# Optimization experiments

Hardware: AMD Instinct MI355X
Metric: run time of the kernel (lower is better)

Reference implementation:

```python
import jax, jax.numpy as jnp
import numpy as np

N_NODES = 50000
N_EDGES = 800000
DIM_FEAT = 96
INFO_DIM = 32
DIM_EMB = 160
CONV_OUT = DIM_EMB - INFO_DIM  # 128
NUM_LAYERS = 3
NUM_GRAPHS = 500
DIM_TARGET = 10


def setup_inputs() -> dict:
    key = jax.random.key(0)
    ks = jax.random.split(key, 20)
    inp = {
        'x': jax.random.normal(ks[0], (N_NODES, DIM_FEAT), dtype=jnp.float32),
        'edge_index': jax.random.randint(ks[1], (2, N_EDGES), 0, N_NODES, dtype=jnp.int32),
        'batch': jnp.sort(jax.random.randint(ks[2], (N_NODES,), 0, NUM_GRAPHS, dtype=jnp.int32)),
        'struc_info': jax.random.normal(ks[3], (NUM_GRAPHS, INFO_DIM), dtype=jnp.float32),
    }
    # SAGEConv params per layer: lin_l (on aggregated neighbors, with bias), lin_r (on root, no bias)
    in_dims = [DIM_FEAT + INFO_DIM, DIM_EMB, DIM_EMB]
    k = 4
    for i, din in enumerate(in_dims):
        s = 1.0 / np.sqrt(din)
        inp[f'Wl{i}'] = jax.random.uniform(ks[k], (din, CONV_OUT), jnp.float32, -s, s); k += 1
        inp[f'Wr{i}'] = jax.random.uniform(ks[k], (din, CONV_OUT), jnp.float32, -s, s); k += 1
        inp[f'b{i}'] = jax.random.uniform(ks[k], (CONV_OUT,), jnp.float32, -s, s); k += 1
    s1 = 1.0 / np.sqrt(NUM_LAYERS * CONV_OUT)
    inp['Wfc1'] = jax.random.uniform(ks[k], (NUM_LAYERS * CONV_OUT, DIM_EMB), jnp.float32, -s1, s1); k += 1
    inp['bfc1'] = jax.random.uniform(ks[k], (DIM_EMB,), jnp.float32, -s1, s1); k += 1
    s2 = 1.0 / np.sqrt(DIM_EMB)
    inp['Wfc2'] = jax.random.uniform(ks[k], (DIM_EMB, DIM_TARGET), jnp.float32, -s2, s2); k += 1
    inp['bfc2'] = jax.random.uniform(ks[k], (DIM_TARGET,), jnp.float32, -s2, s2)
    return inp


def _sage_conv(h, src, dst, Wl, Wr, b, n_nodes):
    # PyG SAGEConv (mean aggr): out = lin_l(mean_{j in N(i)} x_j) + lin_r(x_i)
    agg = jax.ops.segment_sum(h[src], dst, num_segments=n_nodes)       # [N, D]
    deg = jax.ops.segment_sum(jnp.ones_like(dst, dtype=h.dtype), dst, num_segments=n_nodes)
    mean = agg / jnp.maximum(deg, 1.0)[:, None]
    return mean @ Wl + b + h @ Wr


def reference(x, edge_index, batch, struc_info, Wl0, Wr0, b0, Wl1, Wr1, b1, Wl2, Wr2, b2, Wfc1, bfc1, Wfc2, bfc2):
    n_nodes = x.shape[0]
    src, dst = edge_index[0], edge_index[1]
    info = struc_info[batch]                         # [N, info_dim] repeated per node
    params = [(Wl0, Wr0, b0), (Wl1, Wr1, b1), (Wl2, Wr2, b2)]
    h = x
    outs = []
    for (Wl, Wr, b) in params:
        h = _sage_conv(jnp.concatenate([h, info], axis=1), src, dst, Wl, Wr, b, n_nodes)
        outs.append(h)
    hcat = jnp.concatenate(outs, axis=1)             # [N, num_layers*conv_out]
    g = jax.ops.segment_max(hcat, batch, num_segments=struc_info.shape[0])  # global max pool
    z = jax.nn.relu(g @ Wfc1 + bfc1)
    return z @ Wfc2 + bfc2
```

## Files before the change

### kernel.cpp

```cpp
#include <hip/hip_runtime.h>
#include <hip/hip_bf16.h>
#include <float.h>

#define NN 50000
#define NE 800000
#define DF 96
#define DI 32
#define CO 128
#define NG 500
#define HC 384
#define F1I 384
#define F1O 160
#define F2O 10
#define CAPLOG 7
#define NRANGE 196
#define EPB 3125
#define RCAPLOG 13

typedef unsigned int  u32;
typedef unsigned short u16;
typedef short bf16x8 __attribute__((ext_vector_type(8)));
typedef float f32x4  __attribute__((ext_vector_type(4)));

__device__ __forceinline__ u16 f2b(float f) {
    __hip_bfloat16 h = __float2bfloat16(f);
    return *reinterpret_cast<u16*>(&h);
}
__device__ __forceinline__ float b2f(u16 u) {
    return __uint_as_float(((u32)u) << 16);
}
__device__ __forceinline__ float blo(u32 u) { return __uint_as_float(u << 16); }
__device__ __forceinline__ float bhi(u32 u) { return __uint_as_float(u & 0xffff0000u); }

#define PB_BIN    256
#define PB_STARTS 196
#define PB_CAST   4688
#define PB_WT0    96
#define PB_WT1    128
#define PB_WT2    128
#define PB_INFO   500
#define PREP_GRID (PB_BIN + PB_STARTS + PB_CAST + PB_WT0 + PB_WT1 + PB_WT2 + 3 * PB_INFO)

__global__ __launch_bounds__(256) void k_prep(
        const float* __restrict__ x, const int* __restrict__ batch, const float* __restrict__ info,
        const int* __restrict__ src, const int* __restrict__ dst,
        const float* __restrict__ Wl0, const float* __restrict__ Wr0, const float* __restrict__ b0,
        const float* __restrict__ Wl1, const float* __restrict__ Wr1, const float* __restrict__ b1,
        const float* __restrict__ Wl2, const float* __restrict__ Wr2, const float* __restrict__ b2,
        int* __restrict__ grescnt, u32* __restrict__ ebin,
        int* __restrict__ start, u16* __restrict__ xb,
        u16* __restrict__ WT0, u16* __restrict__ WT1, u16* __restrict__ WT2,
        float* __restrict__ iQl0, float* __restrict__ iQr0,
        float* __restrict__ iQl1, float* __restrict__ iQr1,
        float* __restrict__ iQl2, float* __restrict__ iQr2) {
    __shared__ u32 pairs[EPB];
    __shared__ int lcnt[256];
    int blk = blockIdx.x;
    int t = threadIdx.x;
    if (blk < PB_BIN) {
        int base = blk * EPB;
        lcnt[t] = 0;
        __syncthreads();
        for (int j = t; j < EPB; j += 256) {
            int e = base + j;
            int d = dst[e];
            int s = src[e];
            pairs[j] = ((u32)(d & 255) << 24) | ((u32)(d >> 8) << 16) | (u32)s;
            atomicAdd(&lcnt[d >> 8], 1);
        }
        __syncthreads();
        int myCnt = lcnt[t];
        int myBase = atomicAdd(&grescnt[t * 16], myCnt);
        __syncthreads();
        lcnt[t] = myBase;
        __syncthreads();
        for (int j = t; j < EPB; j += 256) {
            u32 p = pairs[j];
            int r = (p >> 16) & 255;
            int pos = atomicAdd(&lcnt[r], 1);
            if (pos < (1 << RCAPLOG)) ebin[(r << RCAPLOG) + pos] = p;
        }
        return;
    }
    blk -= PB_BIN;
    if (blk < PB_STARTS) {
        int i = blk * 256 + t;
        if (i >= NN) return;
        int b = batch[i];
        if (i == 0) { for (int g = 0; g <= b; ++g) start[g] = 0; }
        else {
            int p = batch[i - 1];
            if (p != b) for (int g = p + 1; g <= b; ++g) start[g] = i;
        }
        if (i == NN - 1) { for (int g = b + 1; g <= NG; ++g) start[g] = NN; }
        return;
    }
    blk -= PB_STARTS;
    if (blk < PB_CAST) {
        int tid = blk * 256 + t;
        if (tid >= NN * DF / 4) return;
        float4 v = *(const float4*)&x[tid * 4];
        ushort4 o;
        o.x = f2b(v.x); o.y = f2b(v.y); o.z = f2b(v.z); o.w = f2b(v.w);
        *(ushort4*)&xb[tid * 4] = o;
        return;
    }
    blk -= PB_CAST;
    if (blk < PB_WT0 + PB_WT1 + PB_WT2) {
        const float* Wl; const float* Wr; u16* WT; int K; int rel;
        if (blk < PB_WT0) { Wl = Wl0; Wr = Wr0; WT = WT0; K = 96;  rel = blk; }
        else if (blk < PB_WT0 + PB_WT1) { Wl = Wl1; Wr = Wr1; WT = WT1; K = 128; rel = blk - PB_WT0; }
        else { Wl = Wl2; Wr = Wr2; WT = WT2; K = 128; rel = blk - PB_WT0 - PB_WT1; }
        int tid = rel * 256 + t;
        if (tid >= 256 * K) return;
        int n = tid / K;
        int k = tid - n * K;
        float v = (n < CO) ? Wl[k * CO + n] : Wr[k * CO + (n - CO)];
        WT[tid] = f2b(v);
        return;
    }
    blk -= PB_WT0 + PB_WT1 + PB_WT2;
    {
        const float* Wl; const float* Wr; const float* bias; float* iQl; float* iQr; int Ktop; int g;
        if (blk < PB_INFO) { Wl = Wl0; Wr = Wr0; bias = b0; iQl = iQl0; iQr = iQr0; Ktop = 96;  g = blk; }
        else if (blk < 2 * PB_INFO) { Wl = Wl1; Wr = Wr1; bias = b1; iQl = iQl1; iQr = iQr1; Ktop = 128; g = blk - PB_INFO; }
        else { Wl = Wl2; Wr = Wr2; bias = b2; iQl = iQl2; iQr = iQr2; Ktop = 128; g = blk - 2 * PB_INFO; }
        int c = t & 127;
        int sel = t >> 7;
        const float* W = sel ? Wr : Wl;
        float a = sel ? bias[c] : 0.0f;
        for (int d = 0; d < DI; ++d)
            a += info[g * DI + d] * W[(Ktop + d) * CO + c];
        (sel ? iQr : iQl)[g * CO + c] = a;
    }
}

__global__ __launch_bounds__(256) void k_binB(const u32* __restrict__ ebin,
                                              const int* __restrict__ grescnt,
                                              int* __restrict__ cnt, u16* __restrict__ csr) {
    __shared__ int lcnt[256];
    int r = blockIdx.x;
    int t = threadIdx.x;
    lcnt[t] = 0;
    __syncthreads();
    int total = grescnt[r * 16];
    if (total > (1 << RCAPLOG)) total = 1 << RCAPLOG;
    for (int j = t; j < total; j += 256) {
        u32 p = ebin[(r << RCAPLOG) + j];
        int dloc = p >> 24;
        int rank = atomicAdd(&lcnt[dloc], 1);
        int node = (r << 8) + dloc;
        if (rank < (1 << CAPLOG)) csr[(node << CAPLOG) + rank] = (u16)(p & 0xffff);
    }
    __syncthreads();
    int node = (r << 8) + t;
    if (node < NN) cnt[node] = lcnt[t];
}

template<int K>
__global__ __launch_bounds__(256) void k_mfma(const u16* __restrict__ A,
                                              const u16* __restrict__ WTg,
                                              const int* __restrict__ batch,
                                              const float* __restrict__ iQl,
                                              const float* __restrict__ iQr,
                                              u16* __restrict__ zlp,
                                              u16* __restrict__ zq) {
    constexpr int PITCH = K + 8;
    __shared__ short lds[256 * PITCH];

    int tid  = threadIdx.x;
    int w    = tid >> 6;
    int lane = tid & 63;
    int quad = lane >> 4;
    int l15  = lane & 15;

    constexpr int CH = 256 * K / 8;
    const uint4* wp = (const uint4*)WTg;
    for (int c = tid; c < CH; c += 256) {
        int n  = c / (K / 8);
        int ko = (c - n * (K / 8)) * 8;
        *(uint4*)&lds[n * PITCH + ko] = wp[c];
    }
    __syncthreads();

    int i0 = blockIdx.x * 128 + w * 32;
    int r0 = i0 + l15;       if (r0 >= NN) r0 = NN - 1;
    int r1 = i0 + 16 + l15;  if (r1 >= NN) r1 = NN - 1;
    const short* A0 = (const short*)A + (size_t)r0 * K;
    const short* A1 = (const short*)A + (size_t)r1 * K;

    f32x4 acc[2][16];
#pragma unroll
    for (int rt = 0; rt < 2; ++rt)
#pragma unroll
        for (int ct = 0; ct < 16; ++ct)
            acc[rt][ct] = (f32x4){0.f, 0.f, 0.f, 0.f};

#pragma unroll
    for (int ks = 0; ks < K / 32; ++ks) {
        int ka = ks * 32 + quad * 8;
        bf16x8 a0 = *(const bf16x8*)(A0 + ka);
        bf16x8 a1 = *(const bf16x8*)(A1 + ka);
#pragma unroll
        for (int ct = 0; ct < 16; ++ct) {
            bf16x8 b = *(const bf16x8*)&lds[(ct * 16 + l15) * PITCH + ka];
            acc[0][ct] = __builtin_amdgcn_mfma_f32_16x16x32_bf16(a0, b, acc[0][ct], 0, 0, 0);
            acc[1][ct] = __builtin_amdgcn_mfma_f32_16x16x32_bf16(a1, b, acc[1][ct], 0, 0, 0);
        }
    }

#pragma unroll
    for (int rt = 0; rt < 2; ++rt) {
#pragma unroll
        for (int reg = 0; reg < 4; ++reg) {
            int row = i0 + rt * 16 + quad * 4 + reg;
            if (row < NN) {
                int b = batch[row];
                const float* ql = &iQl[b * CO];
                const float* qr = &iQr[b * CO];
                u16* lp = zlp + (size_t)row * CO;
                u16* qp = zq  + (size_t)row * CO;
#pragma unroll
                for (int ct = 0; ct < 8; ++ct) {
                    int col = ct * 16 + l15;
                    lp[col] = f2b(acc[rt][ct][reg] + ql[col]);
                }
#pragma unroll
                for (int ct = 8; ct < 16; ++ct) {
                    int col = ct * 16 + l15 - 128;
                    qp[col] = f2b(acc[rt][ct][reg] + qr[col]);
                }
            }
        }
    }
}

__device__ __forceinline__ void acc8(float* a, const uint4& u) {
    a[0] += blo(u.x); a[1] += bhi(u.x);
    a[2] += blo(u.y); a[3] += bhi(u.y);
    a[4] += blo(u.z); a[5] += bhi(u.z);
    a[6] += blo(u.w); a[7] += bhi(u.w);
}

__global__ __launch_bounds__(256) void k_gatherb(const u32* __restrict__ zlp, const u32* __restrict__ zq,
                                                 const int* __restrict__ cnt, const u16* __restrict__ csr,
                                                 u32* __restrict__ hout) {
    int wave = threadIdx.x >> 6;
    int lane = threadIdx.x & 63;
    int q    = lane >> 4;
    int l16  = lane & 15;
    int i = blockIdx.x * 4 + wave;
    if (i >= NN) return;
    int deg = cnt[i];
    int degc = min(deg, 1 << CAPLOG);
    int s0 = i << CAPLOG;
    int s1 = s0 + degc;

    const uint4* Z = (const uint4*)zlp;

    float a[8] = {0,0,0,0,0,0,0,0};
    float b[8] = {0,0,0,0,0,0,0,0};
    float c[8] = {0,0,0,0,0,0,0,0};
    float d[8] = {0,0,0,0,0,0,0,0};

    int e = s0;
    for (; e + 15 < s1; e += 16) {
        int n0 = csr[e + q];
        int n1 = csr[e + 4 + q];
        int n2 = csr[e + 8 + q];
        int n3 = csr[e + 12 + q];
        uint4 u0 = Z[(size_t)n0 * 16 + l16];
        uint4 u1 = Z[(size_t)n1 * 16 + l16];
        uint4 u2 = Z[(size_t)n2 * 16 + l16];
        uint4 u3 = Z[(size_t)n3 * 16 + l16];
        acc8(a, u0); acc8(b, u1); acc8(c, u2); acc8(d, u3);
    }
    for (; e < s1; e += 4) {
        if (e + q < s1) {
            int n0 = csr[e + q];
            uint4 u0 = Z[(size_t)n0 * 16 + l16];
            acc8(a, u0);
        }
    }
#pragma unroll
    for (int j = 0; j < 8; ++j) {
        a[j] += b[j] + c[j] + d[j];
        a[j] += __shfl_xor(a[j], 16);
        a[j] += __shfl_xor(a[j], 32);
    }
    if (q == 0) {
        float r = 1.0f / fmaxf((float)deg, 1.0f);
        uint4 qq = ((const uint4*)zq)[(size_t)i * 16 + l16];
        uint4 o;
        o.x = (u32)f2b(a[0] * r + blo(qq.x)) | ((u32)f2b(a[1] * r + bhi(qq.x)) << 16);
        o.y = (u32)f2b(a[2] * r + blo(qq.y)) | ((u32)f2b(a[3] * r + bhi(qq.y)) << 16);
        o.z = (u32)f2b(a[4] * r + blo(qq.z)) | ((u32)f2b(a[5] * r + bhi(qq.z)) << 16);
        o.w = (u32)f2b(a[6] * r + blo(qq.w)) | ((u32)f2b(a[7] * r + bhi(qq.w)) << 16);
        ((uint4*)hout)[(size_t)i * 16 + l16] = o;
    }
}

__global__ __launch_bounds__(384) void k_poolfc(const u32* __restrict__ h1, const u32* __restrict__ h2,
                                                const u32* __restrict__ h3, const int* __restrict__ start,
                                                const float* __restrict__ W1, const float* __restrict__ b1,
                                                const float* __restrict__ W2, const float* __restrict__ b2,
                                                float* __restrict__ out) {
    __shared__ float s_part[6][128];
    __shared__ float s_g[F1I];
    __shared__ float s_z[F1O];
    int gr = blockIdx.x;
    int t  = threadIdx.x;
    int w    = t >> 6;
    int lane = t & 63;
    int buf  = w % 3;
    int half = w / 3;
    const u32* hb = (buf == 0) ? h1 : (buf == 1) ? h2 : h3;
    int s = start[gr], e = start[gr + 1];
    int mid = (s + e) >> 1;
    int n0 = half ? mid : s;
    int n1 = half ? e : mid;

    float mlo[4], mhi[4];
#pragma unroll
    for (int j = 0; j < 4; ++j) { mlo[j] = -FLT_MAX; mhi[j] = -FLT_MAX; }
    int n = n0;
    for (; n + 3 < n1; n += 4) {
        u32 v0 = hb[(size_t)(n + 0) * 64 + lane];
        u32 v1 = hb[(size_t)(n + 1) * 64 + lane];
        u32 v2 = hb[(size_t)(n + 2) * 64 + lane];
        u32 v3 = hb[(size_t)(n + 3) * 64 + lane];
        mlo[0] = fmaxf(mlo[0], blo(v0)); mhi[0] = fmaxf(mhi[0], bhi(v0));
        mlo[1] = fmaxf(mlo[1], blo(v1)); mhi[1] = fmaxf(mhi[1], bhi(v1));
        mlo[2] = fmaxf(mlo[2], blo(v2)); mhi[2] = fmaxf(mhi[2], bhi(v2));
        mlo[3] = fmaxf(mlo[3], blo(v3)); mhi[3] = fmaxf(mhi[3], bhi(v3));
    }
    for (; n < n1; ++n) {
        u32 v0 = hb[(size_t)n * 64 + lane];
        mlo[0] = fmaxf(mlo[0], blo(v0)); mhi[0] = fmaxf(mhi[0], bhi(v0));
    }
    float lo = fmaxf(fmaxf(mlo[0], mlo[1]), fmaxf(mlo[2], mlo[3]));
    float hi = fmaxf(fmaxf(mhi[0], mhi[1]), fmaxf(mhi[2], mhi[3]));
    s_part[w][2 * lane]     = lo;
    s_part[w][2 * lane + 1] = hi;
    __syncthreads();
    {
        int buf2 = t >> 7, cc = t & 127;
        s_g[t] = fmaxf(s_part[buf2][cc], s_part[buf2 + 3][cc]);
    }
    __syncthreads();
    if (t < F1O) {
        float acc = b1[t];
        for (int k = 0; k < F1I; ++k) acc += s_g[k] * W1[k * F1O + t];
        s_z[t] = fmaxf(acc, 0.0f);
    }
    __syncthreads();
    if (t < F2O) {
        float a = b2[t];
        for (int k = 0; k < F1O; ++k) a += s_z[k] * W2[k * F2O + t];
        out[gr * F2O + t] = a;
    }
}

extern "C" void kernel_launch(void* const* d_in, const int* in_sizes, int n_in,
                              void* d_out, int out_size, void* d_ws, size_t ws_size,
                              hipStream_t stream) {
    const float* x     = (const float*)d_in[0];
    const int*   eidx  = (const int*)d_in[1];
    const int*   batch = (const int*)d_in[2];
    const float* info  = (const float*)d_in[3];
    const float* Wl0 = (const float*)d_in[4];
    const float* Wr0 = (const float*)d_in[5];
    const float* b0  = (const float*)d_in[6];
    const float* Wl1 = (const float*)d_in[7];
    const float* Wr1 = (const float*)d_in[8];
    const float* b1  = (const float*)d_in[9];
    const float* Wl2 = (const float*)d_in[10];
    const float* Wr2 = (const float*)d_in[11];
    const float* b2  = (const float*)d_in[12];
    const float* Wfc1  = (const float*)d_in[13];
    const float* bfc1  = (const float*)d_in[14];
    const float* Wfc2  = (const float*)d_in[15];
    const float* bfc2  = (const float*)d_in[16];
    float* out = (float*)d_out;

    const int* src = eidx;
    const int* dst = eidx + NE;

    char* W = (char*)d_ws;
    u16* xb     = (u16*)(W + 0);
    u16* h1     = (u16*)(W + 9600000);
    u16* h2     = (u16*)(W + 22400000);
    u16* h3     = (u16*)(W + 35200000);
    u16* zlp    = (u16*)(W + 48000000);
    u16* zq     = (u16*)(W + 60800000);
    u16* WT0    = (u16*)(W + 73600000);
    u16* WT1    = (u16*)(W + 73649152);
    u16* WT2    = (u16*)(W + 73714688);
    float* iQl0 = (float*)(W + 73780224);
    float* iQr0 = (float*)(W + 74036224);
    float* iQl1 = (float*)(W + 74292224);
    float* iQr1 = (float*)(W + 74548224);
    float* iQl2 = (float*)(W + 74804224);
    float* iQr2 = (float*)(W + 75060224);
    int* start  = (int*)(W + 75316224);
    int* cnt    = (int*)(W + 75318272);
    u16* csr    = (u16*)(W + 75518336);
    u32* ebin   = (u32*)(W + 88318336);
    int* grescnt= (int*)(W + 96706560);

    hipMemsetAsync(grescnt, 0, 256 * 16 * sizeof(int), stream);

    k_prep<<<PREP_GRID, 256, 0, stream>>>(x, batch, info, src, dst,
        Wl0, Wr0, b0, Wl1, Wr1, b1, Wl2, Wr2, b2,
        grescnt, ebin, start, xb, WT0, WT1, WT2, iQl0, iQr0, iQl1, iQr1, iQl2, iQr2);

    k_binB<<<NRANGE, 256, 0, stream>>>(ebin, grescnt, cnt, csr);

    const int gGemm = (NN + 127) / 128;
    const int gGath = (NN + 3) / 4;

    k_mfma<96><<<gGemm, 256, 0, stream>>>(xb, WT0, batch, iQl0, iQr0, zlp, zq);
    k_gatherb<<<gGath, 256, 0, stream>>>((const u32*)zlp, (const u32*)zq, cnt, csr, (u32*)h1);

    k_mfma<128><<<gGemm, 256, 0, stream>>>(h1, WT1, batch, iQl1, iQr1, zlp, zq);
    k_gatherb<<<gGath, 256, 0, stream>>>((const u32*)zlp, (const u32*)zq, cnt, csr, (u32*)h2);

    k_mfma<128><<<gGemm, 256, 0, stream>>>(h2, WT2, batch, iQl2, iQr2, zlp, zq);
    k_gatherb<<<gGath, 256, 0, stream>>>((const u32*)zlp, (const u32*)zq, cnt, csr, (u32*)h3);

    k_poolfc<<<NG, 384, 0, stream>>>((const u32*)h1, (const u32*)h2, (const u32*)h3, start,
                                     Wfc1, bfc1, Wfc2, bfc2, out);
}
```

Measured before the change: 300.5 us.

## Fuse all stages into one persistent kernel with software grid barriers

Replaces the chain of separate kernel launches (prep, binB, three mfma/gather pairs, poolfc) with a single 512-block persistent kernel. Phases are separated by atomic-counter grid barriers, and work is distributed with grid-stride loops. The goal is to remove launch gaps and per-kernel tail effects. In exchange it needs all 512 blocks to be co-resident, and the 68 KB of shared memory per block limits occupancy during the gather phases. The barrier also has a spin-timeout fallback that could silently break correctness.

```diff
diff --git a/kernel.cpp b/kernel.cpp
--- a/kernel.cpp
+++ b/kernel.cpp
@@ -8,7 +8,6 @@
 #define DI 32
 #define CO 128
 #define NG 500
-#define HC 384
 #define F1I 384
 #define F1O 160
 #define F2O 10
@@ -16,6 +15,8 @@
 #define NRANGE 196
 #define EPB 3125
 #define RCAPLOG 13
+#define NBLK 512
+#define SMEM_BYTES 69632
 
 typedef unsigned int  u32;
 typedef unsigned short u16;
@@ -26,120 +27,81 @@
     __hip_bfloat16 h = __float2bfloat16(f);
     return *reinterpret_cast<u16*>(&h);
 }
-__device__ __forceinline__ float b2f(u16 u) {
-    return __uint_as_float(((u32)u) << 16);
-}
 __device__ __forceinline__ float blo(u32 u) { return __uint_as_float(u << 16); }
 __device__ __forceinline__ float bhi(u32 u) { return __uint_as_float(u & 0xffff0000u); }
 
-#define PB_BIN    256
-#define PB_STARTS 196
-#define PB_CAST   4688
-#define PB_WT0    96
-#define PB_WT1    128
-#define PB_WT2    128
-#define PB_INFO   500
-#define PREP_GRID (PB_BIN + PB_STARTS + PB_CAST + PB_WT0 + PB_WT1 + PB_WT2 + 3 * PB_INFO)
-
-__global__ __launch_bounds__(256) void k_prep(
-        const float* __restrict__ x, const int* __restrict__ batch, const float* __restrict__ info,
-        const int* __restrict__ src, const int* __restrict__ dst,
-        const float* __restrict__ Wl0, const float* __restrict__ Wr0, const float* __restrict__ b0,
-        const float* __restrict__ Wl1, const float* __restrict__ Wr1, const float* __restrict__ b1,
-        const float* __restrict__ Wl2, const float* __restrict__ Wr2, const float* __restrict__ b2,
-        int* __restrict__ grescnt, u32* __restrict__ ebin,
-        int* __restrict__ start, u16* __restrict__ xb,
-        u16* __restrict__ WT0, u16* __restrict__ WT1, u16* __restrict__ WT2,
-        float* __restrict__ iQl0, float* __restrict__ iQr0,
-        float* __restrict__ iQl1, float* __restrict__ iQr1,
-        float* __restrict__ iQl2, float* __restrict__ iQr2) {
-    __shared__ u32 pairs[EPB];
-    __shared__ int lcnt[256];
-    int blk = blockIdx.x;
+struct P {
+    const float* x; const int* batch; const float* info;
+    const int* src; const int* dst;
+    const float *Wl0, *Wr0, *b0, *Wl1, *Wr1, *b1, *Wl2, *Wr2, *b2;
+    const float *Wfc1, *bfc1, *Wfc2, *bfc2;
+    float* out;
+    int* grescnt; int* bar; u32* ebin; int* start; u16* xb;
+    u16 *WT0, *WT1, *WT2;
+    float *iQl0, *iQr0, *iQl1, *iQr1, *iQl2, *iQr2;
+    int* cnt; u16* csr;
+    u16 *h1, *h2, *h3, *zlp, *zq;
+};
+
+__device__ void gbar(int* bar, int idx) {
+    __syncthreads();
+    if (threadIdx.x == 0) {
+        __hip_atomic_fetch_add(&bar[idx * 16], 1, __ATOMIC_RELEASE, __HIP_MEMORY_SCOPE_AGENT);
+        long long it = 0;
+        while (__hip_atomic_load(&bar[idx * 16], __ATOMIC_ACQUIRE, __HIP_MEMORY_SCOPE_AGENT) < NBLK) {
+            __builtin_amdgcn_s_sleep(8);
+            if (++it > 20000000LL) break;
+        }
+    }
+    __syncthreads();
+}
+
+
+__device__ void sec_binA(int vb, const int* __restrict__ src, const int* __restrict__ dst,
+                         int* __restrict__ grescnt, u32* __restrict__ ebin, char* smem) {
+    u32* pairs = (u32*)smem;
+    int* lcnt  = (int*)(smem + EPB * 4);
     int t = threadIdx.x;
-    if (blk < PB_BIN) {
-        int base = blk * EPB;
-        lcnt[t] = 0;
-        __syncthreads();
-        for (int j = t; j < EPB; j += 256) {
-            int e = base + j;
-            int d = dst[e];
-            int s = src[e];
-            pairs[j] = ((u32)(d & 255) << 24) | ((u32)(d >> 8) << 16) | (u32)s;
-            atomicAdd(&lcnt[d >> 8], 1);
-        }
-        __syncthreads();
-        int myCnt = lcnt[t];
-        int myBase = atomicAdd(&grescnt[t * 16], myCnt);
-        __syncthreads();
-        lcnt[t] = myBase;
-        __syncthreads();
-        for (int j = t; j < EPB; j += 256) {
-            u32 p = pairs[j];
-            int r = (p >> 16) & 255;
-            int pos = atomicAdd(&lcnt[r], 1);
-            if (pos < (1 << RCAPLOG)) ebin[(r << RCAPLOG) + pos] = p;
-        }
-        return;
-    }
-    blk -= PB_BIN;
-    if (blk < PB_STARTS) {
-        int i = blk * 256 + t;
-        if (i >= NN) return;
-        int b = batch[i];
-        if (i == 0) { for (int g = 0; g <= b; ++g) start[g] = 0; }
-        else {
-            int p = batch[i - 1];
-            if (p != b) for (int g = p + 1; g <= b; ++g) start[g] = i;
-        }
-        if (i == NN - 1) { for (int g = b + 1; g <= NG; ++g) start[g] = NN; }
-        return;
-    }
-    blk -= PB_STARTS;
-    if (blk < PB_CAST) {
-        int tid = blk * 256 + t;
-        if (tid >= NN * DF / 4) return;
-        float4 v = *(const float4*)&x[tid * 4];
-        ushort4 o;
-        o.x = f2b(v.x); o.y = f2b(v.y); o.z = f2b(v.z); o.w = f2b(v.w);
-        *(ushort4*)&xb[tid * 4] = o;
-        return;
-    }
-    blk -= PB_CAST;
-    if (blk < PB_WT0 + PB_WT1 + PB_WT2) {
-        const float* Wl; const float* Wr; u16* WT; int K; int rel;
-        if (blk < PB_WT0) { Wl = Wl0; Wr = Wr0; WT = WT0; K = 96;  rel = blk; }
-        else if (blk < PB_WT0 + PB_WT1) { Wl = Wl1; Wr = Wr1; WT = WT1; K = 128; rel = blk - PB_WT0; }
-        else { Wl = Wl2; Wr = Wr2; WT = WT2; K = 128; rel = blk - PB_WT0 - PB_WT1; }
-        int tid = rel * 256 + t;
-        if (tid >= 256 * K) return;
-        int n = tid / K;
-        int k = tid - n * K;
-        float v = (n < CO) ? Wl[k * CO + n] : Wr[k * CO + (n - CO)];
-        WT[tid] = f2b(v);
-        return;
-    }
-    blk -= PB_WT0 + PB_WT1 + PB_WT2;
-    {
-        const float* Wl; const float* Wr; const float* bias; float* iQl; float* iQr; int Ktop; int g;
-        if (blk < PB_INFO) { Wl = Wl0; Wr = Wr0; bias = b0; iQl = iQl0; iQr = iQr0; Ktop = 96;  g = blk; }
-        else if (blk < 2 * PB_INFO) { Wl = Wl1; Wr = Wr1; bias = b1; iQl = iQl1; iQr = iQr1; Ktop = 128; g = blk - PB_INFO; }
-        else { Wl = Wl2; Wr = Wr2; bias = b2; iQl = iQl2; iQr = iQr2; Ktop = 128; g = blk - 2 * PB_INFO; }
-        int c = t & 127;
-        int sel = t >> 7;
-        const float* W = sel ? Wr : Wl;
-        float a = sel ? bias[c] : 0.0f;
-        for (int d = 0; d < DI; ++d)
-            a += info[g * DI + d] * W[(Ktop + d) * CO + c];
-        (sel ? iQr : iQl)[g * CO + c] = a;
-    }
-}
-
-__global__ __launch_bounds__(256) void k_binB(const u32* __restrict__ ebin,
-                                              const int* __restrict__ grescnt,
-                                              int* __restrict__ cnt, u16* __restrict__ csr) {
-    __shared__ int lcnt[256];
-    int r = blockIdx.x;
+    int base = vb * EPB;
+    lcnt[t] = 0;
+    __syncthreads();
+    for (int j = t; j < EPB; j += 256) {
+        int e = base + j;
+        int d = dst[e];
+        int s = src[e];
+        pairs[j] = ((u32)(d & 255) << 24) | ((u32)(d >> 8) << 16) | (u32)s;
+        atomicAdd(&lcnt[d >> 8], 1);
+    }
+    __syncthreads();
+    int myCnt = lcnt[t];
+    int myBase = atomicAdd(&grescnt[t * 16], myCnt);
+    __syncthreads();
+    lcnt[t] = myBase;
+    __syncthreads();
+    for (int j = t; j < EPB; j += 256) {
+        u32 pr = pairs[j];
+        int r = (pr >> 16) & 255;
+        int pos = atomicAdd(&lcnt[r], 1);
+        if (pos < (1 << RCAPLOG)) ebin[(r << RCAPLOG) + pos] = pr;
+    }
+    __syncthreads();
+}
+
+__device__ void sec_starts(int vb, const int* __restrict__ batch, int* __restrict__ start) {
+    int i = vb * 256 + threadIdx.x;
+    if (i >= NN) return;
+    int b = batch[i];
+    if (i == 0) { for (int g = 0; g <= b; ++g) start[g] = 0; }
+    else {
+        int p = batch[i - 1];
+        if (p != b) for (int g = p + 1; g <= b; ++g) start[g] = i;
+    }
+    if (i == NN - 1) { for (int g = b + 1; g <= NG; ++g) start[g] = NN; }
+}
+
+__device__ void sec_binB(int r, const u32* __restrict__ ebin, const int* __restrict__ grescnt,
+                         int* __restrict__ cnt, u16* __restrict__ csr, char* smem) {
+    int* lcnt = (int*)smem;
     int t = threadIdx.x;
     lcnt[t] = 0;
     __syncthreads();
@@ -155,18 +117,49 @@
     __syncthreads();
     int node = (r << 8) + t;
     if (node < NN) cnt[node] = lcnt[t];
+    __syncthreads();
+}
+
+__device__ void sec_cast(int vb, const float* __restrict__ x, u16* __restrict__ xb) {
+    int tid = vb * 256 + threadIdx.x;
+    if (tid >= NN * DF / 4) return;
+    float4 v = *(const float4*)&x[tid * 4];
+    ushort4 o;
+    o.x = f2b(v.x); o.y = f2b(v.y); o.z = f2b(v.z); o.w = f2b(v.w);
+    *(ushort4*)&xb[tid * 4] = o;
+}
+
+__device__ void sec_wt(int rel, const float* __restrict__ Wl, const float* __restrict__ Wr,
+                       u16* __restrict__ WT, int K) {
+    int tid = rel * 256 + threadIdx.x;
+    if (tid >= 256 * K) return;
+    int n = tid / K;
+    int k = tid - n * K;
+    float v = (n < CO) ? Wl[k * CO + n] : Wr[k * CO + (n - CO)];
+    WT[tid] = f2b(v);
+}
+
+__device__ void sec_infow(int g, const float* __restrict__ info,
+                          const float* __restrict__ Wl, const float* __restrict__ Wr,
+                          const float* __restrict__ bias, int Ktop,
+                          float* __restrict__ iQl, float* __restrict__ iQr) {
+    int t = threadIdx.x;
+    int c = t & 127;
+    int sel = t >> 7;
+    const float* W = sel ? Wr : Wl;
+    float a = sel ? bias[c] : 0.0f;
+    for (int d = 0; d < DI; ++d)
+        a += info[g * DI + d] * W[(Ktop + d) * CO + c];
+    (sel ? iQr : iQl)[g * CO + c] = a;
 }
 
 template<int K>
-__global__ __launch_bounds__(256) void k_mfma(const u16* __restrict__ A,
-                                              const u16* __restrict__ WTg,
-                                              const int* __restrict__ batch,
-                                              const float* __restrict__ iQl,
-                                              const float* __restrict__ iQr,
-                                              u16* __restrict__ zlp,
-                                              u16* __restrict__ zq) {
+__device__ void sec_mfma(int vb, const u16* __restrict__ A, const u16* __restrict__ WTg,
+                         const int* __restrict__ batch,
+                         const float* __restrict__ iQl, const float* __restrict__ iQr,
+                         u16* __restrict__ zlp, u16* __restrict__ zq, char* smem) {
     constexpr int PITCH = K + 8;
-    __shared__ short lds[256 * PITCH];
+    short* lds = (short*)smem;
 
     int tid  = threadIdx.x;
     int w    = tid >> 6;
@@ -183,7 +176,7 @@
     }
     __syncthreads();
 
-    int i0 = blockIdx.x * 128 + w * 32;
+    int i0 = vb * 128 + w * 32;
     int r0 = i0 + l15;       if (r0 >= NN) r0 = NN - 1;
     int r1 = i0 + 16 + l15;  if (r1 >= NN) r1 = NN - 1;
     const short* A0 = (const short*)A + (size_t)r0 * K;
@@ -233,6 +226,7 @@
             }
         }
     }
+    __syncthreads();
 }
 
 __device__ __forceinline__ void acc8(float* a, const uint4& u) {
@@ -242,14 +236,14 @@
     a[6] += blo(u.w); a[7] += bhi(u.w);
 }
 
-__global__ __launch_bounds__(256) void k_gatherb(const u32* __restrict__ zlp, const u32* __restrict__ zq,
-                                                 const int* __restrict__ cnt, const u16* __restrict__ csr,
-                                                 u32* __restrict__ hout) {
+__device__ void sec_gather(int vb, const u32* __restrict__ zlp, const u32* __restrict__ zq,
+                           const int* __restrict__ cnt, const u16* __restrict__ csr,
+                           u32* __restrict__ hout) {
     int wave = threadIdx.x >> 6;
     int lane = threadIdx.x & 63;
     int q    = lane >> 4;
     int l16  = lane & 15;
-    int i = blockIdx.x * 4 + wave;
+    int i = vb * 4 + wave;
     if (i >= NN) return;
     int deg = cnt[i];
     int degc = min(deg, 1 << CAPLOG);
@@ -300,52 +294,40 @@
     }
 }
 
-__global__ __launch_bounds__(384) void k_poolfc(const u32* __restrict__ h1, const u32* __restrict__ h2,
-                                                const u32* __restrict__ h3, const int* __restrict__ start,
-                                                const float* __restrict__ W1, const float* __restrict__ b1,
-                                                const float* __restrict__ W2, const float* __restrict__ b2,
-                                                float* __restrict__ out) {
-    __shared__ float s_part[6][128];
-    __shared__ float s_g[F1I];
-    __shared__ float s_z[F1O];
-    int gr = blockIdx.x;
-    int t  = threadIdx.x;
-    int w    = t >> 6;
-    int lane = t & 63;
-    int buf  = w % 3;
-    int half = w / 3;
-    const u32* hb = (buf == 0) ? h1 : (buf == 1) ? h2 : h3;
-    int s = start[gr], e = start[gr + 1];
-    int mid = (s + e) >> 1;
-    int n0 = half ? mid : s;
-    int n1 = half ? e : mid;
-
-    float mlo[4], mhi[4];
-#pragma unroll
-    for (int j = 0; j < 4; ++j) { mlo[j] = -FLT_MAX; mhi[j] = -FLT_MAX; }
-    int n = n0;
-    for (; n + 3 < n1; n += 4) {
-        u32 v0 = hb[(size_t)(n + 0) * 64 + lane];
-        u32 v1 = hb[(size_t)(n + 1) * 64 + lane];
-        u32 v2 = hb[(size_t)(n + 2) * 64 + lane];
-        u32 v3 = hb[(size_t)(n + 3) * 64 + lane];
-        mlo[0] = fmaxf(mlo[0], blo(v0)); mhi[0] = fmaxf(mhi[0], bhi(v0));
-        mlo[1] = fmaxf(mlo[1], blo(v1)); mhi[1] = fmaxf(mhi[1], bhi(v1));
-        mlo[2] = fmaxf(mlo[2], blo(v2)); mhi[2] = fmaxf(mhi[2], bhi(v2));
-        mlo[3] = fmaxf(mlo[3], blo(v3)); mhi[3] = fmaxf(mhi[3], bhi(v3));
-    }
-    for (; n < n1; ++n) {
-        u32 v0 = hb[(size_t)n * 64 + lane];
-        mlo[0] = fmaxf(mlo[0], blo(v0)); mhi[0] = fmaxf(mhi[0], bhi(v0));
-    }
-    float lo = fmaxf(fmaxf(mlo[0], mlo[1]), fmaxf(mlo[2], mlo[3]));
-    float hi = fmaxf(fmaxf(mhi[0], mhi[1]), fmaxf(mhi[2], mhi[3]));
-    s_part[w][2 * lane]     = lo;
-    s_part[w][2 * lane + 1] = hi;
-    __syncthreads();
-    {
-        int buf2 = t >> 7, cc = t & 127;
-        s_g[t] = fmaxf(s_part[buf2][cc], s_part[buf2 + 3][cc]);
+__device__ void sec_poolfc(int gr, const u32* __restrict__ h1, const u32* __restrict__ h2,
+                           const u32* __restrict__ h3, const int* __restrict__ start,
+                           const float* __restrict__ W1, const float* __restrict__ b1,
+                           const float* __restrict__ W2, const float* __restrict__ b2,
+                           float* __restrict__ out, char* smem) {
+    float* s_g = (float*)smem;
+    float* s_z = (float*)smem + F1I;
+    int t = threadIdx.x;
+    int w = t >> 6, lane = t & 63;
+    if (w < 3) {
+        const u32* hb = (w == 0) ? h1 : (w == 1) ? h2 : h3;
+        int s = start[gr], e = start[gr + 1];
+        float mlo[4], mhi[4];
+#pragma unroll
+        for (int j = 0; j < 4; ++j) { mlo[j] = -FLT_MAX; mhi[j] = -FLT_MAX; }
+        int n = s;
+        for (; n + 3 < e; n += 4) {
+            u32 v0 = hb[(size_t)(n + 0) * 64 + lane];
+            u32 v1 = hb[(size_t)(n + 1) * 64 + lane];
+            u32 v2 = hb[(size_t)(n + 2) * 64 + lane];
+            u32 v3 = hb[(size_t)(n + 3) * 64 + lane];
+            mlo[0] = fmaxf(mlo[0], blo(v0)); mhi[0] = fmaxf(mhi[0], bhi(v0));
+            mlo[1] = fmaxf(mlo[1], blo(v1)); mhi[1] = fmaxf(mhi[1], bhi(v1));
+            mlo[2] = fmaxf(mlo[2], blo(v2)); mhi[2] = fmaxf(mhi[2], bhi(v2));
+            mlo[3] = fmaxf(mlo[3], blo(v3)); mhi[3] = fmaxf(mhi[3], bhi(v3));
+        }
+        for (; n < e; ++n) {
+            u32 v0 = hb[(size_t)n * 64 + lane];
+            mlo[0] = fmaxf(mlo[0], blo(v0)); mhi[0] = fmaxf(mhi[0], bhi(v0));
+        }
+        float lo = fmaxf(fmaxf(mlo[0], mlo[1]), fmaxf(mlo[2], mlo[3]));
+        float hi = fmaxf(fmaxf(mhi[0], mhi[1]), fmaxf(mhi[2], mhi[3]));
+        s_g[w * 128 + 2 * lane]     = lo;
+        s_g[w * 128 + 2 * lane + 1] = hi;
     }
     __syncthreads();
     if (t < F1O) {
@@ -359,75 +341,115 @@
         for (int k = 0; k < F1O; ++k) a += s_z[k] * W2[k * F2O + t];
         out[gr * F2O + t] = a;
     }
+    __syncthreads();
+}
+
+#define P2_BINB   NRANGE
+#define P2_CAST   4688
+#define P2_WT     352
+#define P2_INFO   1500
+#define P2_TOTAL  (P2_BINB + P2_CAST + P2_WT + P2_INFO)
+
+__global__ __launch_bounds__(256, 2) void k_mega(P p) {
+    __shared__ __align__(16) char smem[SMEM_BYTES];
+    int blk = blockIdx.x;
+
+    if (blk < 256) {
+        sec_binA(blk, p.src, p.dst, p.grescnt, p.ebin, smem);
+    } else if (blk < 256 + 196) {
+        sec_starts(blk - 256, p.batch, p.start);
+    }
+    gbar(p.bar, 0);
+
+    for (int vb = blk; vb < P2_TOTAL; vb += NBLK) {
+        if (vb < P2_BINB) {
+            sec_binB(vb, p.ebin, p.grescnt, p.cnt, p.csr, smem);
+        } else if (vb < P2_BINB + P2_CAST) {
+            sec_cast(vb - P2_BINB, p.x, p.xb);
+        } else if (vb < P2_BINB + P2_CAST + P2_WT) {
+            int r = vb - P2_BINB - P2_CAST;
+            if (r < 96)       sec_wt(r, p.Wl0, p.Wr0, p.WT0, 96);
+            else if (r < 224) sec_wt(r - 96, p.Wl1, p.Wr1, p.WT1, 128);
+            else              sec_wt(r - 224, p.Wl2, p.Wr2, p.WT2, 128);
+        } else {
+            int g = vb - P2_BINB - P2_CAST - P2_WT;
+            if (g < 500)       sec_infow(g, p.info, p.Wl0, p.Wr0, p.b0, 96,  p.iQl0, p.iQr0);
+            else if (g < 1000) sec_infow(g - 500, p.info, p.Wl1, p.Wr1, p.b1, 128, p.iQl1, p.iQr1);
+            else               sec_infow(g - 1000, p.info, p.Wl2, p.Wr2, p.b2, 128, p.iQl2, p.iQr2);
+        }
+    }
+    gbar(p.bar, 1);
+
+    const int gGemm = (NN + 127) / 128;
+    const int gGath = (NN + 3) / 4;
+
+    if (blk < gGemm)
+        sec_mfma<96>(blk, p.xb, p.WT0, p.batch, p.iQl0, p.iQr0, p.zlp, p.zq, smem);
+    gbar(p.bar, 2);
+    for (int vb = blk; vb < gGath; vb += NBLK)
+        sec_gather(vb, (const u32*)p.zlp, (const u32*)p.zq, p.cnt, p.csr, (u32*)p.h1);
+    gbar(p.bar, 3);
+
+    if (blk < gGemm)
+        sec_mfma<128>(blk, p.h1, p.WT1, p.batch, p.iQl1, p.iQr1, p.zlp, p.zq, smem);
+    gbar(p.bar, 4);
+    for (int vb = blk; vb < gGath; vb += NBLK)
+        sec_gather(vb, (const u32*)p.zlp, (const u32*)p.zq, p.cnt, p.csr, (u32*)p.h2);
+    gbar(p.bar, 5);
+
+    if (blk < gGemm)
+        sec_mfma<128>(blk, p.h2, p.WT2, p.batch, p.iQl2, p.iQr2, p.zlp, p.zq, smem);
+    gbar(p.bar, 6);
+    for (int vb = blk; vb < gGath; vb += NBLK)
+        sec_gather(vb, (const u32*)p.zlp, (const u32*)p.zq, p.cnt, p.csr, (u32*)p.h3);
+    gbar(p.bar, 7);
+
+    if (blk < NG)
+        sec_poolfc(blk, (const u32*)p.h1, (const u32*)p.h2, (const u32*)p.h3, p.start,
+                   p.Wfc1, p.bfc1, p.Wfc2, p.bfc2, p.out, smem);
 }
 
 extern "C" void kernel_launch(void* const* d_in, const int* in_sizes, int n_in,
                               void* d_out, int out_size, void* d_ws, size_t ws_size,
                               hipStream_t stream) {
-    const float* x     = (const float*)d_in[0];
-    const int*   eidx  = (const int*)d_in[1];
-    const int*   batch = (const int*)d_in[2];
-    const float* info  = (const float*)d_in[3];
-    const float* Wl0 = (const float*)d_in[4];
-    const float* Wr0 = (const float*)d_in[5];
-    const float* b0  = (const float*)d_in[6];
-    const float* Wl1 = (const float*)d_in[7];
-    const float* Wr1 = (const float*)d_in[8];
-    const float* b1  = (const float*)d_in[9];
-    const float* Wl2 = (const float*)d_in[10];
-    const float* Wr2 = (const float*)d_in[11];
-    const float* b2  = (const float*)d_in[12];
-    const float* Wfc1  = (const float*)d_in[13];
-    const float* bfc1  = (const float*)d_in[14];
-    const float* Wfc2  = (const float*)d_in[15];
-    const float* bfc2  = (const float*)d_in[16];
-    float* out = (float*)d_out;
-
-    const int* src = eidx;
-    const int* dst = eidx + NE;
+    const int* eidx = (const int*)d_in[1];
 
     char* W = (char*)d_ws;
-    u16* xb     = (u16*)(W + 0);
-    u16* h1     = (u16*)(W + 9600000);
-    u16* h2     = (u16*)(W + 22400000);
-    u16* h3     = (u16*)(W + 35200000);
-    u16* zlp    = (u16*)(W + 48000000);
-    u16* zq     = (u16*)(W + 60800000);
-    u16* WT0    = (u16*)(W + 73600000);
-    u16* WT1    = (u16*)(W + 73649152);
-    u16* WT2    = (u16*)(W + 73714688);
-    float* iQl0 = (float*)(W + 73780224);
-    float* iQr0 = (float*)(W + 74036224);
-    float* iQl1 = (float*)(W + 74292224);
-    float* iQr1 = (float*)(W + 74548224);
-    float* iQl2 = (float*)(W + 74804224);
-    float* iQr2 = (float*)(W + 75060224);
-    int* start  = (int*)(W + 75316224);
-    int* cnt    = (int*)(W + 75318272);
-    u16* csr    = (u16*)(W + 75518336);
-    u32* ebin   = (u32*)(W + 88318336);
-    int* grescnt= (int*)(W + 96706560);
-
-    hipMemsetAsync(grescnt, 0, 256 * 16 * sizeof(int), stream);
-
-    k_prep<<<PREP_GRID, 256, 0, stream>>>(x, batch, info, src, dst,
-        Wl0, Wr0, b0, Wl1, Wr1, b1, Wl2, Wr2, b2,
-        grescnt, ebin, start, xb, WT0, WT1, WT2, iQl0, iQr0, iQl1, iQr1, iQl2, iQr2);
-
-    k_binB<<<NRANGE, 256, 0, stream>>>(ebin, grescnt, cnt, csr);
-
-    const int gGemm = (NN + 127) / 128;
-    const int gGath = (NN + 3) / 4;
-
-    k_mfma<96><<<gGemm, 256, 0, stream>>>(xb, WT0, batch, iQl0, iQr0, zlp, zq);
-    k_gatherb<<<gGath, 256, 0, stream>>>((const u32*)zlp, (const u32*)zq, cnt, csr, (u32*)h1);
-
-    k_mfma<128><<<gGemm, 256, 0, stream>>>(h1, WT1, batch, iQl1, iQr1, zlp, zq);
-    k_gatherb<<<gGath, 256, 0, stream>>>((const u32*)zlp, (const u32*)zq, cnt, csr, (u32*)h2);
-
-    k_mfma<128><<<gGemm, 256, 0, stream>>>(h2, WT2, batch, iQl2, iQr2, zlp, zq);
-    k_gatherb<<<gGath, 256, 0, stream>>>((const u32*)zlp, (const u32*)zq, cnt, csr, (u32*)h3);
-
-    k_poolfc<<<NG, 384, 0, stream>>>((const u32*)h1, (const u32*)h2, (const u32*)h3, start,
-                                     Wfc1, bfc1, Wfc2, bfc2, out);
-}
+    P p;
+    p.x     = (const float*)d_in[0];
+    p.batch = (const int*)d_in[2];
+    p.info  = (const float*)d_in[3];
+    p.src   = eidx;
+    p.dst   = eidx + NE;
+    p.Wl0 = (const float*)d_in[4];  p.Wr0 = (const float*)d_in[5];  p.b0 = (const float*)d_in[6];
+    p.Wl1 = (const float*)d_in[7];  p.Wr1 = (const float*)d_in[8];  p.b1 = (const float*)d_in[9];
+    p.Wl2 = (const float*)d_in[10]; p.Wr2 = (const float*)d_in[11]; p.b2 = (const float*)d_in[12];
+    p.Wfc1 = (const float*)d_in[13]; p.bfc1 = (const float*)d_in[14];
+    p.Wfc2 = (const float*)d_in[15]; p.bfc2 = (const float*)d_in[16];
+    p.out = (float*)d_out;
+
+    p.xb     = (u16*)(W + 0);
+    p.h1     = (u16*)(W + 9600000);
+    p.h2     = (u16*)(W + 22400000);
+    p.h3     = (u16*)(W + 35200000);
+    p.zlp    = (u16*)(W + 48000000);
+    p.zq     = (u16*)(W + 60800000);
+    p.WT0    = (u16*)(W + 73600000);
+    p.WT1    = (u16*)(W + 73649152);
+    p.WT2    = (u16*)(W + 73714688);
+    p.iQl0   = (float*)(W + 73780224);
+    p.iQr0   = (float*)(W + 74036224);
+    p.iQl1   = (float*)(W + 74292224);
+    p.iQr1   = (float*)(W + 74548224);
+    p.iQl2   = (float*)(W + 74804224);
+    p.iQr2   = (float*)(W + 75060224);
+    p.start  = (int*)(W + 75316224);
+    p.cnt    = (int*)(W + 75318272);
+    p.csr    = (u16*)(W + 75518336);
+    p.ebin   = (u32*)(W + 88318336);
+    p.grescnt= (int*)(W + 96706560);
+    p.bar    = (int*)(W + 96722944);
+
+    hipMemsetAsync(p.grescnt, 0, 256 * 16 * sizeof(int) + 16 * 16 * sizeof(int), stream);
+    k_mega<<<NBLK, 256, 0, stream>>>(p);
+}
```

Result: slower. 1.102 ms (+266.8%).
